# Kernel tuning notes

Hardware: AMD Instinct MI355X
Metric: run time of the kernel (lower is better)

The kernel has to match this reference:

```python
import jax, jax.numpy as jnp
import numpy as np

B, L, C = 2, 2048, 1024
H, HD = 16, 64
MAX_SCALE_MUL = float(np.log(100.0))
SCALE = 1.0  # attn_l2_norm=True -> scale is 1


def setup_inputs() -> dict:
    key = jax.random.key(0)
    ks = jax.random.split(key, 6)
    x = jax.random.normal(ks[0], (B, L, C), dtype=jnp.float32)
    attn_bias = jax.random.normal(ks[1], (1, 1, L, L), dtype=jnp.float32)
    w_qkv = jax.random.normal(ks[2], (3 * C, C), dtype=jnp.float32) * (1.0 / np.sqrt(C))
    q_bias = jnp.zeros((C,), dtype=jnp.float32)
    v_bias = jnp.zeros((C,), dtype=jnp.float32)
    scale_mul = jnp.full((1, H, 1, 1), np.log(4.0), dtype=jnp.float32)  # scale_mul_1H11
    w_proj = jax.random.normal(ks[3], (C, C), dtype=jnp.float32) * (1.0 / np.sqrt(C))
    b_proj = jnp.zeros((C,), dtype=jnp.float32)
    return {"x": x, "attn_bias": attn_bias, "w_qkv": w_qkv, "q_bias": q_bias,
            "v_bias": v_bias, "scale_mul": scale_mul, "w_proj": w_proj, "b_proj": b_proj}


def reference(x, attn_bias, w_qkv, q_bias, v_bias, scale_mul, w_proj, b_proj):
    # qkv projection with concatenated bias (q_bias, zeros, v_bias)
    bias = jnp.concatenate([q_bias, jnp.zeros_like(q_bias), v_bias])  # [3C]
    qkv = jnp.einsum('blc,dc->bld', x, w_qkv) + bias                  # [B,L,3C]
    qkv = qkv.reshape(B, L, 3, H, HD).transpose(2, 0, 3, 1, 4)        # [3,B,H,L,HD]
    q, k, v = qkv[0], qkv[1], qkv[2]
    # attn_l2_norm path: L2-normalize q,k; q scaled by exp(clamped scale_mul)
    sm = jnp.exp(jnp.minimum(scale_mul, MAX_SCALE_MUL))               # [1,H,1,1]
    q = q / jnp.linalg.norm(q, axis=-1, keepdims=True) * sm
    k = k / jnp.linalg.norm(k, axis=-1, keepdims=True)
    # slow_attn: scaled scores + bias, softmax, weighted sum
    attn = jnp.einsum('bhld,bhmd->bhlm', q * SCALE, k) + attn_bias    # [B,H,L,L]
    p = jax.nn.softmax(attn, axis=-1)
    oup = jnp.einsum('bhlm,bhmd->bhld', p, v)                         # [B,H,L,HD]
    oup = oup.transpose(0, 2, 1, 3).reshape(B, L, C)
    return jnp.einsum('blc,dc->bld', oup, w_proj) + b_proj
```

## Files before the change

### kernel.cpp

```cpp
#include <hip/hip_runtime.h>
#include <cstdint>
#include <cstddef>
#include <math.h>

typedef __attribute__((ext_vector_type(8))) __bf16 bf16x8;
typedef __attribute__((ext_vector_type(4))) __bf16 bf16x4;
typedef __attribute__((ext_vector_type(4))) float f32x4;

#define AS1 __attribute__((address_space(1)))
#define AS3 __attribute__((address_space(3)))

#define LOG2E 1.4426950408889634f

__device__ __forceinline__ void gld16(void* lds_uniform, const void* gaddr) {
  __builtin_amdgcn_global_load_lds((const AS1 unsigned int*)gaddr,
                                   (AS3 unsigned int*)lds_uniform, 16, 0, 0);
}

__global__ __launch_bounds__(256)
void cvt_all_kernel(const float* __restrict__ x, const float* __restrict__ wqkv,
                    const float* __restrict__ wproj,
                    __bf16* __restrict__ xb, __bf16* __restrict__ wqkvb,
                    __bf16* __restrict__ wprojb) {
  const int b = blockIdx.x;
  const float* src; __bf16* dst; int off;
  if (b < 4096)      { src = x;     dst = xb;     off = b; }
  else if (b < 7168) { src = wqkv;  dst = wqkvb;  off = b - 4096; }
  else               { src = wproj; dst = wprojb; off = b - 7168; }
  const int i = (off * 256 + threadIdx.x) * 4;
  const float4 v = *(const float4*)(src + i);
  bf16x4 o;
  o[0] = (__bf16)v.x; o[1] = (__bf16)v.y; o[2] = (__bf16)v.z; o[3] = (__bf16)v.w;
  *(bf16x4*)(dst + i) = o;
}

__global__ __launch_bounds__(256, 2)
void gemm_qkv_kernel(const __bf16* __restrict__ A, const __bf16* __restrict__ B,
                     const float* __restrict__ q_bias, const float* __restrict__ v_bias,
                     const float* __restrict__ scale_mul,
                     __bf16* __restrict__ qb, __bf16* __restrict__ ktp, __bf16* __restrict__ vb) {
  __shared__ __attribute__((aligned(16))) __bf16 As[128 * 32];
  __shared__ __attribute__((aligned(16))) __bf16 Bs[128 * 32];
  const int tid = threadIdx.x;
  const int w = tid >> 6, lane = tid & 63;
  const int m0 = blockIdx.y * 128, n0 = blockIdx.x * 128;
  const int wm = (w >> 1) * 64, wn = (w & 1) * 64;
  const int c = lane & 15, g = lane >> 4;
  f32x4 acc[4][4];
#pragma unroll
  for (int i = 0; i < 4; ++i)
#pragma unroll
    for (int j = 0; j < 4; ++j) acc[i][j] = (f32x4)(0.0f);

  const int r_row = lane >> 2;
  const int r_col = (lane & 3) * 16;
  const char* Abase = (const char*)A + (size_t)m0 * 2048;
  const char* Bbase = (const char*)B + (size_t)n0 * 2048;

  for (int kt = 0; kt < 1024; kt += 32) {
#pragma unroll
    for (int s = 0; s < 2; ++s) {
      const int R = w * 2 + s;
      const int row = R * 16 + r_row;
      gld16((char*)As + R * 1024, Abase + (size_t)row * 2048 + kt * 2 + r_col);
      gld16((char*)Bs + R * 1024, Bbase + (size_t)row * 2048 + kt * 2 + r_col);
    }
    __syncthreads();
    bf16x8 af[4], bfr[4];
#pragma unroll
    for (int i = 0; i < 4; ++i) {
      af[i]  = *(const bf16x8*)((const char*)As + (wm + i * 16 + c) * 64 + g * 16);
      bfr[i] = *(const bf16x8*)((const char*)Bs + (wn + i * 16 + c) * 64 + g * 16);
    }
#pragma unroll
    for (int ni = 0; ni < 4; ++ni)
#pragma unroll
      for (int mi = 0; mi < 4; ++mi)
        acc[ni][mi] = __builtin_amdgcn_mfma_f32_16x16x32_bf16(bfr[ni], af[mi], acc[ni][mi], 0, 0, 0);
    __syncthreads();
  }

  const int nbase = n0 + wn;
  const int which = nbase >> 10;
  const int h = (nbase >> 6) & 15;
  float smh = 1.0f;
  if (which == 0) smh = __expf(fminf(scale_mul[h], 4.605170185988091f)) * LOG2E;
  float4 cb[4];
#pragma unroll
  for (int ni = 0; ni < 4; ++ni) {
    if (which == 0)      cb[ni] = *(const float4*)(q_bias + nbase + ni * 16 + 4 * g);
    else if (which == 2) cb[ni] = *(const float4*)(v_bias + nbase - 2048 + ni * 16 + 4 * g);
    else                 cb[ni] = make_float4(0.f, 0.f, 0.f, 0.f);
  }
  const int mrow0 = m0 + wm;
  const int b2 = mrow0 >> 11;
  const int lpos0 = mrow0 & 2047;
  __bf16* kt_tile = ktp + (size_t)(b2 * 16 + h) * 131072 + (size_t)(lpos0 >> 6) * 4096;
  __bf16* dst_qv = ((which == 0) ? qb : vb) + ((size_t)((b2 * 16 + h) * 2048 + lpos0)) * 64;

#pragma unroll
  for (int mi = 0; mi < 4; ++mi) {
    float v[4][4];
    float ss = 0.0f;
#pragma unroll
    for (int ni = 0; ni < 4; ++ni) {
      v[ni][0] = acc[ni][mi][0] + cb[ni].x;
      v[ni][1] = acc[ni][mi][1] + cb[ni].y;
      v[ni][2] = acc[ni][mi][2] + cb[ni].z;
      v[ni][3] = acc[ni][mi][3] + cb[ni].w;
#pragma unroll
      for (int j = 0; j < 4; ++j) ss += v[ni][j] * v[ni][j];
    }
    ss += __shfl_xor(ss, 16, 64);
    ss += __shfl_xor(ss, 32, 64);
    const float sc = (which == 2) ? 1.0f : (rsqrtf(ss) * smh);
    const int key = mi * 16 + c;
    if (which == 1) {
#pragma unroll
      for (int ni = 0; ni < 4; ++ni) {
        bf16x4 pk;
        pk[0] = (__bf16)(v[ni][0] * sc); pk[1] = (__bf16)(v[ni][1] * sc);
        pk[2] = (__bf16)(v[ni][2] * sc); pk[3] = (__bf16)(v[ni][3] * sc);
        *(bf16x4*)(kt_tile + (ni >> 1) * 2048 + key * 32 + (ni & 1) * 16 + 4 * g) = pk;
      }
    } else {
      __bf16* drow = dst_qv + (size_t)key * 64;
#pragma unroll
      for (int ni = 0; ni < 4; ++ni) {
        bf16x4 pk;
        pk[0] = (__bf16)(v[ni][0] * sc); pk[1] = (__bf16)(v[ni][1] * sc);
        pk[2] = (__bf16)(v[ni][2] * sc); pk[3] = (__bf16)(v[ni][3] * sc);
        *(bf16x4*)(drow + ni * 16 + 4 * g) = pk;
      }
    }
  }
}

__global__ __launch_bounds__(256)
void vtrans_kernel(const __bf16* __restrict__ vb, __bf16* __restrict__ vtp) {
  __shared__ __attribute__((aligned(16))) __bf16 Vs[4][64 * 64];
  const int w = threadIdx.x >> 6, lane = threadIdx.x & 63;
  const int idx = blockIdx.x * 4 + w;
  const int bh = idx >> 5, tile = idx & 31;
  const __bf16* src = vb + ((size_t)bh * 2048 + tile * 64) * 64;
#pragma unroll
  for (int s = 0; s < 8; ++s)
    gld16((char*)&Vs[w][0] + s * 1024, (const char*)src + s * 1024 + lane * 16);
  __syncthreads();
  __bf16* outb = vtp + (size_t)idx * 4096;
#pragma unroll
  for (int r = 0; r < 8; ++r) {
    const int o = r * 512 + lane * 8;
    const int hd = (o >> 5) & 63;
    const int sl0 = ((o >> 11) << 5) | (o & 31);
    bf16x8 pk;
#pragma unroll
    for (int i = 0; i < 8; ++i) {
      const int slot = sl0 + i;
      const int key = (slot & 3) * 16 + (slot >> 2);
      pk[i] = Vs[w][key * 64 + hd];
    }
    *(bf16x8*)(outb + o) = pk;
  }
}

__global__ __launch_bounds__(256)
void btrans_kernel(const float* __restrict__ bias, __bf16* __restrict__ btr) {
  __shared__ __bf16 T[32][264];
  const int tid = threadIdx.x;
  const int rb = blockIdx.x >> 3, cg = blockIdx.x & 7;
  const float* src = bias + (size_t)(rb * 32) * 2048 + cg * 256;
#pragma unroll
  for (int i = 0; i < 8; ++i) {
    const int u = i * 256 + tid;
    const int r = u >> 6, c4 = (u & 63) * 4;
    const float4 v = *(const float4*)(src + (size_t)r * 2048 + c4);
    T[r][c4 + 0] = (__bf16)(v.x * LOG2E);
    T[r][c4 + 1] = (__bf16)(v.y * LOG2E);
    T[r][c4 + 2] = (__bf16)(v.z * LOG2E);
    T[r][c4 + 3] = (__bf16)(v.w * LOG2E);
  }
  __syncthreads();
  const int ktl = tid >> 6;
  const int lane = tid & 63, g = lane >> 4, c = lane & 15;
  __bf16 outv[32];
#pragma unroll
  for (int v = 0; v < 32; ++v) {
    const int mi = v >> 4, ni = (v >> 2) & 3, j = v & 3;
    outv[v] = T[mi * 16 + g * 4 + j][ktl * 64 + ni * 16 + c];
  }
  __bf16* dst = btr + ((size_t)(rb * 32 + cg * 4 + ktl) * 64 + lane) * 32;
#pragma unroll
  for (int i = 0; i < 4; ++i)
    *(bf16x8*)(dst + i * 8) = *(bf16x8*)(outv + i * 8);
}

#define STAGE(t, b) {                                                          \
  const char* _ks = kp + (size_t)(t) * 8192 + w * 2048 + lane * 16;            \
  const char* _vs = vp + (size_t)(t) * 8192 + w * 2048 + lane * 16;            \
  gld16(&Kb[b][w * 2048],        _ks);                                         \
  gld16(&Kb[b][w * 2048 + 1024], _ks + 1024);                                  \
  gld16(&Vb[b][w * 2048],        _vs);                                         \
  gld16(&Vb[b][w * 2048 + 1024], _vs + 1024);                                  \
}

#define COMPUTE(t, b) {                                                        \
  bf16x8 kf[4][2];                                                             \
  _Pragma("unroll")                                                            \
  for (int ni = 0; ni < 4; ++ni)                                               \
    _Pragma("unroll")                                                          \
    for (int ks = 0; ks < 2; ++ks)                                             \
      kf[ni][ks] = *(const bf16x8*)(&Kb[b][0] + ks * 4096 + (ni * 16 + c) * 64 + g * 16); \
  f32x4 sacc[2][4];                                                            \
  _Pragma("unroll")                                                            \
  for (int mi = 0; mi < 2; ++mi)                                               \
    _Pragma("unroll")                                                          \
    for (int ni = 0; ni < 4; ++ni) {                                           \
      f32x4 s_ = __builtin_amdgcn_mfma_f32_16x16x32_bf16(qf[mi][0], kf[ni][0], (f32x4)(0.0f), 0, 0, 0); \
      sacc[mi][ni] = __builtin_amdgcn_mfma_f32_16x16x32_bf16(qf[mi][1], kf[ni][1], s_, 0, 0, 0); \
    }                                                                          \
  const char* _bb = bp + ((size_t)(t) * 64 + lane) * 64;                       \
  bf16x8 bA[4];                                                                \
  _Pragma("unroll")                                                            \
  for (int i = 0; i < 4; ++i) bA[i] = *(const bf16x8*)(_bb + i * 16);          \
  _Pragma("unroll")                                                            \
  for (int mi = 0; mi < 2; ++mi)                                               \
    _Pragma("unroll")                                                          \
    for (int j = 0; j < 4; ++j) {                                              \
      const float p0 = __builtin_amdgcn_exp2f(sacc[mi][0][j] + (float)bA[(mi * 16 + 0 + j) >> 3][(mi * 16 + 0 + j) & 7]);  \
      const float p1 = __builtin_amdgcn_exp2f(sacc[mi][1][j] + (float)bA[(mi * 16 + 4 + j) >> 3][(mi * 16 + 4 + j) & 7]);  \
      const float p2 = __builtin_amdgcn_exp2f(sacc[mi][2][j] + (float)bA[(mi * 16 + 8 + j) >> 3][(mi * 16 + 8 + j) & 7]);  \
      const float p3 = __builtin_amdgcn_exp2f(sacc[mi][3][j] + (float)bA[(mi * 16 + 12 + j) >> 3][(mi * 16 + 12 + j) & 7]);\
      lsum[mi][j] += (p0 + p1) + (p2 + p3);                                    \
      bf16x4 pk;                                                               \
      pk[0] = (__bf16)p0; pk[1] = (__bf16)p1; pk[2] = (__bf16)p2; pk[3] = (__bf16)p3; \
      *(bf16x4*)&Ps[w][c >> 3][mi * 16 + g * 4 + j][(c & 7) * 4] = pk;         \
    }                                                                          \
  bf16x8 pf[2][2];                                                             \
  _Pragma("unroll")                                                            \
  for (int mi = 0; mi < 2; ++mi)                                               \
    _Pragma("unroll")                                                          \
    for (int ks = 0; ks < 2; ++ks)                                             \
      pf[mi][ks] = *(const bf16x8*)&Ps[w][ks][mi * 16 + c][g * 8];             \
  _Pragma("unroll")                                                            \
  for (int ni = 0; ni < 4; ++ni) {                                             \
    const bf16x8 v0 = *(const bf16x8*)(&Vb[b][0] + 0 * 4096 + ni * 1024 + c * 64 + g * 16); \
    const bf16x8 v1 = *(const bf16x8*)(&Vb[b][0] + 1 * 4096 + ni * 1024 + c * 64 + g * 16); \
    _Pragma("unroll")                                                          \
    for (int mi = 0; mi < 2; ++mi) {                                           \
      oacc[mi][ni] = __builtin_amdgcn_mfma_f32_16x16x32_bf16(pf[mi][0], v0, oacc[mi][ni], 0, 0, 0); \
      oacc[mi][ni] = __builtin_amdgcn_mfma_f32_16x16x32_bf16(pf[mi][1], v1, oacc[mi][ni], 0, 0, 0); \
    }                                                                          \
  }                                                                            \
}

__global__ __launch_bounds__(256, 3)
void attn_kernel(const __bf16* __restrict__ qb, const __bf16* __restrict__ ktp,
                 const __bf16* __restrict__ vtp, const __bf16* __restrict__ btr,
                 float* __restrict__ pO, float* __restrict__ pl) {
  __shared__ __attribute__((aligned(16))) char Kb[2][8192];
  __shared__ __attribute__((aligned(16))) char Vb[2][8192];
  __shared__ __attribute__((aligned(16))) __bf16 Ps[4][2][32][32];
  const int tid = threadIdx.x, w = tid >> 6, lane = tid & 63;
  const int c = lane & 15, g = lane >> 4;
  const int idx = blockIdx.x;
  const int bh = idx & 31, rb = (idx >> 5) & 15, half = idx >> 9;
  const __bf16* qh = qb + (size_t)bh * (2048 * 64);
  const char* kp = (const char*)ktp + (size_t)bh * (32 * 8192);
  const char* vp = (const char*)vtp + (size_t)bh * (32 * 8192);
  const int rb32 = rb * 4 + w;
  const char* bp = (const char*)btr + (size_t)rb32 * 131072;
  const int q0 = rb * 128 + w * 32;

  bf16x8 qf[2][2];
#pragma unroll
  for (int mi = 0; mi < 2; ++mi)
#pragma unroll
    for (int ks = 0; ks < 2; ++ks)
      qf[mi][ks] = *(const bf16x8*)(qh + (size_t)(q0 + mi * 16 + c) * 64 + ks * 32 + g * 8);

  f32x4 oacc[2][4];
  float lsum[2][4];
#pragma unroll
  for (int mi = 0; mi < 2; ++mi)
#pragma unroll
    for (int ni = 0; ni < 4; ++ni) oacc[mi][ni] = (f32x4)(0.0f);
#pragma unroll
  for (int mi = 0; mi < 2; ++mi)
#pragma unroll
    for (int j = 0; j < 4; ++j) lsum[mi][j] = 0.0f;

  const int t0 = half * 16;
  STAGE(t0, 0);
  __syncthreads();
#pragma unroll 1
  for (int tt = 0; tt < 16; tt += 2) {
    if (tt + 1 < 16) STAGE(t0 + tt + 1, 1);
    COMPUTE(t0 + tt, 0);
    __syncthreads();
    if (tt + 2 < 16) STAGE(t0 + tt + 2, 0);
    COMPUTE(t0 + tt + 1, 1);
    __syncthreads();
  }

  float* po  = pO + (((size_t)(half * 32 + bh)) * 2048 + q0) * 64;
  float* plp = pl + ((size_t)(half * 32 + bh)) * 2048 + q0;
#pragma unroll
  for (int mi = 0; mi < 2; ++mi)
#pragma unroll
    for (int j = 0; j < 4; ++j) {
      float l = lsum[mi][j];
      l += __shfl_xor(l, 1, 64);
      l += __shfl_xor(l, 2, 64);
      l += __shfl_xor(l, 4, 64);
      l += __shfl_xor(l, 8, 64);
      const int row = mi * 16 + g * 4 + j;
      if (c == 0) plp[row] = l;
#pragma unroll
      for (int ni = 0; ni < 4; ++ni)
        po[row * 64 + ni * 16 + c] = oacc[mi][ni][j];
    }
}

__global__ __launch_bounds__(256)
void combine_kernel(const float* __restrict__ pO, const float* __restrict__ pl,
                    __bf16* __restrict__ oupb) {
  const int rg = blockIdx.x;
  const int bh = rg & 31, qt = rg >> 5;
  const int b2 = bh >> 4, h = bh & 15;
  const int tid = threadIdx.x;
  const int row = qt * 32 + (tid >> 3), hd0 = (tid & 7) * 8;
  const float l = pl[(size_t)bh * 2048 + row] + pl[(size_t)(32 + bh) * 2048 + row];
  const float inv = 1.0f / l;
  const float* p0 = pO + ((size_t)bh * 2048 + row) * 64 + hd0;
  const float* p1 = pO + ((size_t)(32 + bh) * 2048 + row) * 64 + hd0;
  const float4 a0 = *(const float4*)p0;
  const float4 b0 = *(const float4*)(p0 + 4);
  const float4 a1 = *(const float4*)p1;
  const float4 b1 = *(const float4*)(p1 + 4);
  bf16x8 o;
  o[0] = (__bf16)((a0.x + a1.x) * inv); o[1] = (__bf16)((a0.y + a1.y) * inv);
  o[2] = (__bf16)((a0.z + a1.z) * inv); o[3] = (__bf16)((a0.w + a1.w) * inv);
  o[4] = (__bf16)((b0.x + b1.x) * inv); o[5] = (__bf16)((b0.y + b1.y) * inv);
  o[6] = (__bf16)((b0.z + b1.z) * inv); o[7] = (__bf16)((b0.w + b1.w) * inv);
  *(bf16x8*)(oupb + ((size_t)(b2 * 2048 + row) * 16 + h) * 64 + hd0) = o;
}

__global__ __launch_bounds__(256, 2)
void gemm_proj_kernel(const __bf16* __restrict__ A, const __bf16* __restrict__ B,
                      const float* __restrict__ b_proj, float* __restrict__ out) {
  __shared__ __attribute__((aligned(16))) __bf16 As[64 * 32];
  __shared__ __attribute__((aligned(16))) __bf16 Bs[128 * 32];
  const int tid = threadIdx.x;
  const int w = tid >> 6, lane = tid & 63;
  const int c = lane & 15, g = lane >> 4;
  const int m0 = blockIdx.y * 64, n0 = blockIdx.x * 128;
  const int wm = (w >> 1) * 32, wn = (w & 1) * 64;
  f32x4 acc[2][4];
#pragma unroll
  for (int i = 0; i < 2; ++i)
#pragma unroll
    for (int j = 0; j < 4; ++j) acc[i][j] = (f32x4)(0.0f);

  const int r_row = lane >> 2;
  const int r_col = (lane & 3) * 16;
  const char* Abase = (const char*)A + (size_t)m0 * 2048;
  const char* Bbase = (const char*)B + (size_t)n0 * 2048;

  for (int kt = 0; kt < 1024; kt += 32) {
    {
      const int row = w * 16 + r_row;
      gld16((char*)As + w * 1024, Abase + (size_t)row * 2048 + kt * 2 + r_col);
    }
#pragma unroll
    for (int s = 0; s < 2; ++s) {
      const int R = w * 2 + s;
      const int row = R * 16 + r_row;
      gld16((char*)Bs + R * 1024, Bbase + (size_t)row * 2048 + kt * 2 + r_col);
    }
    __syncthreads();
    bf16x8 af[2], bfr[4];
#pragma unroll
    for (int i = 0; i < 2; ++i)
      af[i] = *(const bf16x8*)((const char*)As + (wm + i * 16 + c) * 64 + g * 16);
#pragma unroll
    for (int i = 0; i < 4; ++i)
      bfr[i] = *(const bf16x8*)((const char*)Bs + (wn + i * 16 + c) * 64 + g * 16);
#pragma unroll
    for (int mi = 0; mi < 2; ++mi)
#pragma unroll
      for (int ni = 0; ni < 4; ++ni)
        acc[mi][ni] = __builtin_amdgcn_mfma_f32_16x16x32_bf16(af[mi], bfr[ni], acc[mi][ni], 0, 0, 0);
    __syncthreads();
  }

  float cbias[4];
#pragma unroll
  for (int ni = 0; ni < 4; ++ni) cbias[ni] = b_proj[n0 + wn + ni * 16 + c];
#pragma unroll
  for (int mi = 0; mi < 2; ++mi)
#pragma unroll
    for (int j = 0; j < 4; ++j) {
      const int m = m0 + wm + mi * 16 + g * 4 + j;
      float* orow = out + (size_t)m * 1024 + n0 + wn;
#pragma unroll
      for (int ni = 0; ni < 4; ++ni)
        orow[ni * 16 + c] = acc[mi][ni][j] + cbias[ni];
    }
}

extern "C" void kernel_launch(void* const* d_in, const int* in_sizes, int n_in,
                              void* d_out, int out_size, void* d_ws, size_t ws_size,
                              hipStream_t stream) {
  const float* x         = (const float*)d_in[0];
  const float* attn_bias = (const float*)d_in[1];
  const float* w_qkv     = (const float*)d_in[2];
  const float* q_bias    = (const float*)d_in[3];
  const float* v_bias    = (const float*)d_in[4];
  const float* scale_mul = (const float*)d_in[5];
  const float* w_proj    = (const float*)d_in[6];
  const float* b_proj    = (const float*)d_in[7];
  float* out = (float*)d_out;

  __bf16* xb     = (__bf16*)d_ws;
  __bf16* wqkvb  = xb + 4194304;
  __bf16* wprojb = wqkvb + 3145728;
  __bf16* qb     = wprojb + 1048576;
  __bf16* ktp    = qb + 4194304;
  __bf16* vtp    = ktp + 4194304;
  __bf16* btr    = vtp + 4194304;
  __bf16* vb     = btr + 4194304;
  float*  pO     = (float*)vb;
  float*  pl     = pO + 2 * 32 * 2048 * 64;
  __bf16* oupb   = xb;

  btrans_kernel<<<512, 256, 0, stream>>>(attn_bias, btr);
  cvt_all_kernel<<<8192, 256, 0, stream>>>(x, w_qkv, w_proj, xb, wqkvb, wprojb);

  gemm_qkv_kernel<<<dim3(24, 32), 256, 0, stream>>>(xb, wqkvb, q_bias, v_bias, scale_mul,
                                                    qb, ktp, vb);
  vtrans_kernel<<<256, 256, 0, stream>>>(vb, vtp);
  attn_kernel<<<1024, 256, 0, stream>>>(qb, ktp, vtp, btr, pO, pl);
  combine_kernel<<<2048, 256, 0, stream>>>(pO, pl, oupb);
  gemm_proj_kernel<<<dim3(8, 64), 256, 0, stream>>>(oupb, wprojb, b_proj, out);
}
```

Baseline: 228.4 us.

## Drop split-KV attention, normalize in-kernel, merge prep kernels

The attention kernel now walks all 32 key tiles per block instead of splitting the keys into two halves, so it normalizes by the row sum and writes bf16 output directly. This removes the fp32 partial-output round trip and the separate combine kernel. The bias transpose and the fp32-to-bf16 conversion are merged into one prep launch, and the P scratch buffer rows are padded from 32 to 40 to reduce LDS bank conflicts. The trade-off is half as many attention blocks (512), each running twice as long, which lowers parallelism and tail balance on the GPU.

```diff
diff --git a/kernel.cpp b/kernel.cpp
--- a/kernel.cpp
+++ b/kernel.cpp
@@ -18,20 +18,51 @@
 }
 
 __global__ __launch_bounds__(256)
-void cvt_all_kernel(const float* __restrict__ x, const float* __restrict__ wqkv,
-                    const float* __restrict__ wproj,
-                    __bf16* __restrict__ xb, __bf16* __restrict__ wqkvb,
-                    __bf16* __restrict__ wprojb) {
+void prep_kernel(const float* __restrict__ x, const float* __restrict__ wqkv,
+                 const float* __restrict__ wproj, const float* __restrict__ bias,
+                 __bf16* __restrict__ xb, __bf16* __restrict__ wqkvb,
+                 __bf16* __restrict__ wprojb, __bf16* __restrict__ btr) {
+  __shared__ __bf16 T[32][264];
   const int b = blockIdx.x;
-  const float* src; __bf16* dst; int off;
-  if (b < 4096)      { src = x;     dst = xb;     off = b; }
-  else if (b < 7168) { src = wqkv;  dst = wqkvb;  off = b - 4096; }
-  else               { src = wproj; dst = wprojb; off = b - 7168; }
-  const int i = (off * 256 + threadIdx.x) * 4;
-  const float4 v = *(const float4*)(src + i);
-  bf16x4 o;
-  o[0] = (__bf16)v.x; o[1] = (__bf16)v.y; o[2] = (__bf16)v.z; o[3] = (__bf16)v.w;
-  *(bf16x4*)(dst + i) = o;
+  const int tid = threadIdx.x;
+  if (b < 8192) {
+    const float* src; __bf16* dst; int off;
+    if (b < 4096)      { src = x;     dst = xb;     off = b; }
+    else if (b < 7168) { src = wqkv;  dst = wqkvb;  off = b - 4096; }
+    else               { src = wproj; dst = wprojb; off = b - 7168; }
+    const int i = (off * 256 + tid) * 4;
+    const float4 v = *(const float4*)(src + i);
+    bf16x4 o;
+    o[0] = (__bf16)v.x; o[1] = (__bf16)v.y; o[2] = (__bf16)v.z; o[3] = (__bf16)v.w;
+    *(bf16x4*)(dst + i) = o;
+    return;
+  }
+  const int bb = b - 8192;
+  const int rb = bb >> 3, cg = bb & 7;
+  const float* src = bias + (size_t)(rb * 32) * 2048 + cg * 256;
+#pragma unroll
+  for (int i = 0; i < 8; ++i) {
+    const int u = i * 256 + tid;
+    const int r = u >> 6, c4 = (u & 63) * 4;
+    const float4 v = *(const float4*)(src + (size_t)r * 2048 + c4);
+    T[r][c4 + 0] = (__bf16)(v.x * LOG2E);
+    T[r][c4 + 1] = (__bf16)(v.y * LOG2E);
+    T[r][c4 + 2] = (__bf16)(v.z * LOG2E);
+    T[r][c4 + 3] = (__bf16)(v.w * LOG2E);
+  }
+  __syncthreads();
+  const int ktl = tid >> 6;
+  const int lane = tid & 63, g = lane >> 4, c = lane & 15;
+  __bf16 outv[32];
+#pragma unroll
+  for (int v = 0; v < 32; ++v) {
+    const int mi = v >> 4, ni = (v >> 2) & 3, j = v & 3;
+    outv[v] = T[mi * 16 + g * 4 + j][ktl * 64 + ni * 16 + c];
+  }
+  __bf16* dst = btr + ((size_t)(rb * 32 + cg * 4 + ktl) * 64 + lane) * 32;
+#pragma unroll
+  for (int i = 0; i < 4; ++i)
+    *(bf16x8*)(dst + i * 8) = *(bf16x8*)(outv + i * 8);
 }
 
 __global__ __launch_bounds__(256, 2)
@@ -164,37 +195,6 @@
   }
 }
 
-__global__ __launch_bounds__(256)
-void btrans_kernel(const float* __restrict__ bias, __bf16* __restrict__ btr) {
-  __shared__ __bf16 T[32][264];
-  const int tid = threadIdx.x;
-  const int rb = blockIdx.x >> 3, cg = blockIdx.x & 7;
-  const float* src = bias + (size_t)(rb * 32) * 2048 + cg * 256;
-#pragma unroll
-  for (int i = 0; i < 8; ++i) {
-    const int u = i * 256 + tid;
-    const int r = u >> 6, c4 = (u & 63) * 4;
-    const float4 v = *(const float4*)(src + (size_t)r * 2048 + c4);
-    T[r][c4 + 0] = (__bf16)(v.x * LOG2E);
-    T[r][c4 + 1] = (__bf16)(v.y * LOG2E);
-    T[r][c4 + 2] = (__bf16)(v.z * LOG2E);
-    T[r][c4 + 3] = (__bf16)(v.w * LOG2E);
-  }
-  __syncthreads();
-  const int ktl = tid >> 6;
-  const int lane = tid & 63, g = lane >> 4, c = lane & 15;
-  __bf16 outv[32];
-#pragma unroll
-  for (int v = 0; v < 32; ++v) {
-    const int mi = v >> 4, ni = (v >> 2) & 3, j = v & 3;
-    outv[v] = T[mi * 16 + g * 4 + j][ktl * 64 + ni * 16 + c];
-  }
-  __bf16* dst = btr + ((size_t)(rb * 32 + cg * 4 + ktl) * 64 + lane) * 32;
-#pragma unroll
-  for (int i = 0; i < 4; ++i)
-    *(bf16x8*)(dst + i * 8) = *(bf16x8*)(outv + i * 8);
-}
-
 #define STAGE(t, b) {                                                          \
   const char* _ks = kp + (size_t)(t) * 8192 + w * 2048 + lane * 16;            \
   const char* _vs = vp + (size_t)(t) * 8192 + w * 2048 + lane * 16;            \
@@ -257,20 +257,21 @@
 __global__ __launch_bounds__(256, 3)
 void attn_kernel(const __bf16* __restrict__ qb, const __bf16* __restrict__ ktp,
                  const __bf16* __restrict__ vtp, const __bf16* __restrict__ btr,
-                 float* __restrict__ pO, float* __restrict__ pl) {
+                 __bf16* __restrict__ oupb) {
   __shared__ __attribute__((aligned(16))) char Kb[2][8192];
   __shared__ __attribute__((aligned(16))) char Vb[2][8192];
-  __shared__ __attribute__((aligned(16))) __bf16 Ps[4][2][32][32];
+  __shared__ __attribute__((aligned(16))) __bf16 Ps[4][2][32][40];
   const int tid = threadIdx.x, w = tid >> 6, lane = tid & 63;
   const int c = lane & 15, g = lane >> 4;
   const int idx = blockIdx.x;
-  const int bh = idx & 31, rb = (idx >> 5) & 15, half = idx >> 9;
+  const int bh = idx & 31, rb = idx >> 5;
   const __bf16* qh = qb + (size_t)bh * (2048 * 64);
   const char* kp = (const char*)ktp + (size_t)bh * (32 * 8192);
   const char* vp = (const char*)vtp + (size_t)bh * (32 * 8192);
   const int rb32 = rb * 4 + w;
   const char* bp = (const char*)btr + (size_t)rb32 * 131072;
   const int q0 = rb * 128 + w * 32;
+  const int b2 = bh >> 4, h = bh & 15;
 
   bf16x8 qf[2][2];
 #pragma unroll
@@ -290,21 +291,18 @@
 #pragma unroll
     for (int j = 0; j < 4; ++j) lsum[mi][j] = 0.0f;
 
-  const int t0 = half * 16;
-  STAGE(t0, 0);
+  STAGE(0, 0);
   __syncthreads();
 #pragma unroll 1
-  for (int tt = 0; tt < 16; tt += 2) {
-    if (tt + 1 < 16) STAGE(t0 + tt + 1, 1);
-    COMPUTE(t0 + tt, 0);
-    __syncthreads();
-    if (tt + 2 < 16) STAGE(t0 + tt + 2, 0);
-    COMPUTE(t0 + tt + 1, 1);
-    __syncthreads();
-  }
-
-  float* po  = pO + (((size_t)(half * 32 + bh)) * 2048 + q0) * 64;
-  float* plp = pl + ((size_t)(half * 32 + bh)) * 2048 + q0;
+  for (int tt = 0; tt < 32; tt += 2) {
+    if (tt + 1 < 32) STAGE(tt + 1, 1);
+    COMPUTE(tt, 0);
+    __syncthreads();
+    if (tt + 2 < 32) STAGE(tt + 2, 0);
+    COMPUTE(tt + 1, 1);
+    __syncthreads();
+  }
+
 #pragma unroll
   for (int mi = 0; mi < 2; ++mi)
 #pragma unroll
@@ -314,36 +312,13 @@
       l += __shfl_xor(l, 2, 64);
       l += __shfl_xor(l, 4, 64);
       l += __shfl_xor(l, 8, 64);
-      const int row = mi * 16 + g * 4 + j;
-      if (c == 0) plp[row] = l;
+      const float inv = 1.0f / l;
+      const int qrow = q0 + mi * 16 + g * 4 + j;
+      __bf16* orow = oupb + ((size_t)(b2 * 2048 + qrow) * 16 + h) * 64;
 #pragma unroll
       for (int ni = 0; ni < 4; ++ni)
-        po[row * 64 + ni * 16 + c] = oacc[mi][ni][j];
-    }
-}
-
-__global__ __launch_bounds__(256)
-void combine_kernel(const float* __restrict__ pO, const float* __restrict__ pl,
-                    __bf16* __restrict__ oupb) {
-  const int rg = blockIdx.x;
-  const int bh = rg & 31, qt = rg >> 5;
-  const int b2 = bh >> 4, h = bh & 15;
-  const int tid = threadIdx.x;
-  const int row = qt * 32 + (tid >> 3), hd0 = (tid & 7) * 8;
-  const float l = pl[(size_t)bh * 2048 + row] + pl[(size_t)(32 + bh) * 2048 + row];
-  const float inv = 1.0f / l;
-  const float* p0 = pO + ((size_t)bh * 2048 + row) * 64 + hd0;
-  const float* p1 = pO + ((size_t)(32 + bh) * 2048 + row) * 64 + hd0;
-  const float4 a0 = *(const float4*)p0;
-  const float4 b0 = *(const float4*)(p0 + 4);
-  const float4 a1 = *(const float4*)p1;
-  const float4 b1 = *(const float4*)(p1 + 4);
-  bf16x8 o;
-  o[0] = (__bf16)((a0.x + a1.x) * inv); o[1] = (__bf16)((a0.y + a1.y) * inv);
-  o[2] = (__bf16)((a0.z + a1.z) * inv); o[3] = (__bf16)((a0.w + a1.w) * inv);
-  o[4] = (__bf16)((b0.x + b1.x) * inv); o[5] = (__bf16)((b0.y + b1.y) * inv);
-  o[6] = (__bf16)((b0.z + b1.z) * inv); o[7] = (__bf16)((b0.w + b1.w) * inv);
-  *(bf16x8*)(oupb + ((size_t)(b2 * 2048 + row) * 16 + h) * 64 + hd0) = o;
+        orow[ni * 16 + c] = (__bf16)(oacc[mi][ni][j] * inv);
+    }
 }
 
 __global__ __launch_bounds__(256, 2)
@@ -430,17 +405,12 @@
   __bf16* vtp    = ktp + 4194304;
   __bf16* btr    = vtp + 4194304;
   __bf16* vb     = btr + 4194304;
-  float*  pO     = (float*)vb;
-  float*  pl     = pO + 2 * 32 * 2048 * 64;
   __bf16* oupb   = xb;
 
-  btrans_kernel<<<512, 256, 0, stream>>>(attn_bias, btr);
-  cvt_all_kernel<<<8192, 256, 0, stream>>>(x, w_qkv, w_proj, xb, wqkvb, wprojb);
-
+  prep_kernel<<<8704, 256, 0, stream>>>(x, w_qkv, w_proj, attn_bias, xb, wqkvb, wprojb, btr);
   gemm_qkv_kernel<<<dim3(24, 32), 256, 0, stream>>>(xb, wqkvb, q_bias, v_bias, scale_mul,
                                                     qb, ktp, vb);
   vtrans_kernel<<<256, 256, 0, stream>>>(vb, vtp);
-  attn_kernel<<<1024, 256, 0, stream>>>(qb, ktp, vtp, btr, pO, pl);
-  combine_kernel<<<2048, 256, 0, stream>>>(pO, pl, oupb);
+  attn_kernel<<<512, 256, 0, stream>>>(qb, ktp, vtp, btr, oupb);
   gemm_proj_kernel<<<dim3(8, 64), 256, 0, stream>>>(oupb, wprojb, b_proj, out);
 }
```

Result: no change. 226.0 us (-1.1%).
